# Kernel optimization log

Measured on AMD Instinct MI355X. Metric: run time of the kernel, lower is better.

Reference implementation:

```python
import jax, jax.numpy as jnp
import numpy as np

N, E, D_IN, D_H, D_OUT = 8000, 256000, 128, 128, 64
TEMP = 10.0       # config temperature.value (non-learnable)
WEIGHT = 1.0      # config weight.value (non-learnable)
LN_EPS = 1e-5


def _gcn_conv(x, W, b, src, dst, n):
    # PyG GCNConv: add self loops, sym-normalized aggregation, then bias.
    h = x @ W
    loop = jnp.arange(n)
    s = jnp.concatenate([src, loop])
    d = jnp.concatenate([dst, loop])
    deg = jnp.zeros((n,), h.dtype).at[d].add(1.0)
    dinv = jax.lax.rsqrt(jnp.maximum(deg, 1e-12))
    norm = dinv[s] * dinv[d]                       # [E+N]
    out = jax.ops.segment_sum(h[s] * norm[:, None], d, num_segments=n)
    return out + b


def _entropy_gradient(x, A, temperature, normalize):
    # E_i = 0.5 * sum_j A_ij ||x_i - x_j||^2  (dense adjacency, as in repo)
    sq = jnp.sum(x * x, axis=1)                    # [N]
    Ax = A @ x                                     # [N,d]
    deg = A.sum(axis=1)                            # [N]
    En = 0.5 * (deg * sq + A @ sq - 2.0 * jnp.sum(x * Ax, axis=1))
    if normalize:
        En = En / (jnp.max(En) + 1e-12)
    logits = -En / temperature
    P = jax.nn.softmax(logits)
    logP = jax.nn.log_softmax(logits)
    S = -jnp.sum(P * logP)
    c = P * (logP + S) / temperature               # dS/dE_k
    # dS/dx_i = c_i*(deg_i x_i - (Ax)_i) + (A^T c)_i x_i - (A^T (c*x))_i
    ATc = A.T @ c
    return (c[:, None] * (deg[:, None] * x - Ax)
            + ATc[:, None] * x - A.T @ (c[:, None] * x))


def _layer_norm(x, gamma, beta):
    mu = jnp.mean(x, axis=-1, keepdims=True)
    var = jnp.mean(jnp.square(x - mu), axis=-1, keepdims=True)
    return (x - mu) * jax.lax.rsqrt(var + LN_EPS) * gamma + beta


def setup_inputs() -> dict:
    key = jax.random.key(0)
    ks = jax.random.split(key, 6)
    def w(k, i, o):
        return jax.random.normal(k, (i, o), jnp.float32) / np.sqrt(i).astype(np.float32)
    return {
        "x": jax.random.normal(ks[0], (N, D_IN), jnp.float32),
        "edge_index": jax.random.randint(ks[1], (2, E), 0, N),
        "W1": w(ks[2], D_IN, D_H), "b1": jnp.zeros((D_H,), jnp.float32),
        "W2": w(ks[3], D_H, D_H), "b2": jnp.zeros((D_H,), jnp.float32),
        "W_out": w(ks[4], D_H, D_OUT), "b_out": jnp.zeros((D_OUT,), jnp.float32),
        "ln_gamma": jnp.ones((D_H,), jnp.float32),
        "ln_beta": jnp.zeros((D_H,), jnp.float32),
    }


def reference(x, edge_index, W1, b1, W2, b2, W_out, b_out, ln_gamma, ln_beta):
    n = x.shape[0]
    src, dst = edge_index[0], edge_index[1]
    # dense adjacency (to_dense_adj sums duplicate edges)
    A = jnp.zeros((n, n), x.dtype).at[src, dst].add(1.0)
    for W, b in ((W1, b1), (W2, b2)):
        h = _gcn_conv(x, W, b, src, dst, n)
        eg = jax.lax.stop_gradient(_entropy_gradient(h, A, TEMP, True))
        h = h + WEIGHT * eg
        h = jax.nn.relu(h)
        x = _layer_norm(h, ln_gamma, ln_beta)
    embedding = _gcn_conv(x, W_out, b_out, src, dst, n)
    return embedding
```

## Files before the change

kernel.cpp:

```cpp
#include <hip/hip_runtime.h>
#include <hip/hip_bf16.h>

#define DH 128

static constexpr float TEMP_ = 10.0f;
static constexpr float LN_EPS_ = 1e-5f;

__device__ __forceinline__ unsigned short f2bf(float f) {
  union { float f; unsigned int i; } v; v.f = f;
  unsigned int b = v.i + 0x7FFFu + ((v.i >> 16) & 1u);
  return (unsigned short)(b >> 16);
}
__device__ __forceinline__ float bf2f(unsigned short u) {
  union { unsigned int i; float f; } v; v.i = ((unsigned int)u) << 16; return v.f;
}
__device__ __forceinline__ void dec2(unsigned int u, float& lo, float& hi) {
  union { unsigned int i; float f; } a, b;
  a.i = u << 16; b.i = u & 0xFFFF0000u;
  lo = a.f; hi = b.f;
}
__device__ __forceinline__ void dec8(uint4 u, float* o) {
  dec2(u.x, o[0], o[1]); dec2(u.y, o[2], o[3]);
  dec2(u.z, o[4], o[5]); dec2(u.w, o[6], o[7]);
}
__device__ __forceinline__ unsigned int pack2(float lo, float hi) {
  return (unsigned int)f2bf(lo) | ((unsigned int)f2bf(hi) << 16);
}

__device__ __forceinline__ float grp_sum16(float v) {
  #pragma unroll
  for (int o = 8; o > 0; o >>= 1) v += __shfl_down(v, o, 16);
  return __shfl(v, 0, 16);
}

__device__ __forceinline__ float blkred(float v, bool mx, float* s4) {
  const int t = threadIdx.x;
  #pragma unroll
  for (int o = 32; o > 0; o >>= 1) {
    float u = __shfl_down(v, o, 64);
    v = mx ? fmaxf(v, u) : v + u;
  }
  __syncthreads();
  if ((t & 63) == 0) s4[t >> 6] = v;
  __syncthreads();
  float r = mx ? fmaxf(fmaxf(s4[0], s4[1]), fmaxf(s4[2], s4[3]))
               : (s4[0] + s4[1]) + (s4[2] + s4[3]);
  __syncthreads();
  return r;
}

__global__ __launch_bounds__(256) void k_gemm1_hist(const float* __restrict__ X,
                                                    const float* __restrict__ W,
                                                    unsigned short* __restrict__ Hb,
                                                    const int* __restrict__ ei, int E,
                                                    int* cnt_d, int* cnt_s, int NT) {
  __shared__ float Ws[64 * DH];
  __shared__ float xs[16 * 128];
  const int t = threadIdx.x;
  if ((int)blockIdx.x < NT) {
    const int row0 = blockIdx.x * 16;
    const float4* xg = (const float4*)(X + row0 * 128);
    float4* xs4 = (float4*)xs;
    xs4[t] = xg[t];
    xs4[t + 256] = xg[t + 256];
    const int c = t & 127, rg = t >> 7;
    float acc[8];
    #pragma unroll
    for (int r = 0; r < 8; ++r) acc[r] = 0.f;
    for (int kt = 0; kt < 2; ++kt) {
      __syncthreads();
      for (int i = t; i < 64 * DH; i += 256) Ws[i] = W[kt * 64 * DH + i];
      __syncthreads();
      for (int k = 0; k < 64; ++k) {
        float wv = Ws[k * DH + c];
        #pragma unroll
        for (int r = 0; r < 8; ++r)
          acc[r] += xs[(rg * 8 + r) * 128 + kt * 64 + k] * wv;
      }
    }
    #pragma unroll
    for (int r = 0; r < 8; ++r)
      Hb[(row0 + rg * 8 + r) * DH + c] = f2bf(acc[r]);
  } else {
    const int nb = gridDim.x - NT;
    for (int e = (blockIdx.x - NT) * 256 + t; e < E; e += nb * 256) {
      atomicAdd(&cnt_s[ei[e]], 1);
      atomicAdd(&cnt_d[ei[E + e]], 1);
    }
  }
}

__global__ __launch_bounds__(256) void k_scan_a(const int* __restrict__ cnt_d,
                                                const int* __restrict__ cnt_s,
                                                int* off_d, int* off_s, int* bsum,
                                                float* dinv, float* dego, int n) {
  __shared__ int ws4[4];
  const int t = threadIdx.x;
  const int dir = blockIdx.x >> 5, blk = blockIdx.x & 31;
  const int* cnt = dir ? cnt_s : cnt_d;
  int* off = dir ? off_s : off_d;
  const int NPB = (n + 31) >> 5;
  const int i = blk * NPB + t;
  const bool valid = (t < NPB) && (i < n);
  int tot = valid ? cnt[i] : 0;
  const int lane = t & 63, w = t >> 6;
  int v = tot;
  #pragma unroll
  for (int o = 1; o < 64; o <<= 1) {
    int u = __shfl_up(v, o, 64);
    if (lane >= o) v += u;
  }
  if (lane == 63) ws4[w] = v;
  __syncthreads();
  int wbase = 0;
  #pragma unroll
  for (int k = 0; k < 4; ++k) wbase += (k < w) ? ws4[k] : 0;
  const int excl = wbase + v - tot;
  if (valid) {
    off[i] = excl;
    if (dir == 0) dinv[i] = rsqrtf((float)tot + 1.0f);
    else          dego[i] = (float)tot;
  }
  if (t == 0) {
    int bt = 0;
    #pragma unroll
    for (int k = 0; k < 4; ++k) bt += ws4[k];
    bsum[dir * 32 + blk] = bt;
  }
}

__global__ __launch_bounds__(256) void k_scan_b(int* cnt_d, int* cnt_s,
                                                int* off_d, int* off_s,
                                                const int* __restrict__ bsum, int n) {
  __shared__ int sb;
  const int t = threadIdx.x;
  const int dir = blockIdx.x >> 5, blk = blockIdx.x & 31;
  int* cnt = dir ? cnt_s : cnt_d;
  int* off = dir ? off_s : off_d;
  if (t == 0) {
    int s = 0;
    for (int k = 0; k < blk; ++k) s += bsum[dir * 32 + k];
    sb = s;
  }
  __syncthreads();
  const int bbase = sb;
  const int NPB = (n + 31) >> 5;
  const int i = blk * NPB + t;
  if (t < NPB && i < n) {
    off[i] = bbase + off[i];
    cnt[i] = 0;
  }
  if (t == 1 && blk == 31) {
    int s = 0;
    for (int k = 0; k < 32; ++k) s += bsum[dir * 32 + k];
    off[n] = s;
  }
}

__global__ void k_fill(const int* __restrict__ ei, int E,
                       const int* __restrict__ off_d, const int* __restrict__ off_s,
                       int* cnt_d, int* cnt_s, int* idx_d, int* idx_s) {
  int e = blockIdx.x * blockDim.x + threadIdx.x;
  if (e < E) {
    int s = ei[e], d = ei[E + e];
    int p = atomicAdd(&cnt_d[d], 1);
    idx_d[off_d[d] + p] = s;
    int q = atomicAdd(&cnt_s[s], 1);
    idx_s[off_s[s] + q] = d;
  }
}

__global__ __launch_bounds__(256) void k_conv_agg(const unsigned short* __restrict__ Hb,
                                                  const float* __restrict__ dinv,
                                                  const float* __restrict__ b,
                                                  const int* __restrict__ off_d,
                                                  const int* __restrict__ idx_d,
                                                  float* __restrict__ G,
                                                  unsigned short* __restrict__ Gb,
                                                  float* __restrict__ sq) {
  const int lane = threadIdx.x & 15;
  const int i = blockIdx.x * 16 + (threadIdx.x >> 4);
  const uint4* Hv = (const uint4*)Hb;
  const float di = dinv[i];
  float acc[8];
  {
    float t8[8]; dec8(Hv[i * 16 + lane], t8);
    #pragma unroll
    for (int k = 0; k < 8; ++k) acc[k] = di * t8[k];
  }
  int o = off_d[i];
  const int oe = off_d[i + 1];
  for (; o + 8 <= oe; o += 8) {
    int s[8]; float dv[8]; uint4 r[8];
    #pragma unroll
    for (int j = 0; j < 8; ++j) s[j] = idx_d[o + j];
    #pragma unroll
    for (int j = 0; j < 8; ++j) { r[j] = Hv[s[j] * 16 + lane]; dv[j] = dinv[s[j]]; }
    #pragma unroll
    for (int j = 0; j < 8; ++j) {
      float t8[8]; dec8(r[j], t8);
      #pragma unroll
      for (int k = 0; k < 8; ++k) acc[k] = fmaf(dv[j], t8[k], acc[k]);
    }
  }
  for (; o < oe; ++o) {
    int s = idx_d[o];
    float dvs = dinv[s];
    float t8[8]; dec8(Hv[s * 16 + lane], t8);
    #pragma unroll
    for (int k = 0; k < 8; ++k) acc[k] = fmaf(dvs, t8[k], acc[k]);
  }
  const float4 b0 = ((const float4*)b)[lane * 2];
  const float4 b1 = ((const float4*)b)[lane * 2 + 1];
  float gi[8];
  gi[0] = fmaf(di, acc[0], b0.x); gi[1] = fmaf(di, acc[1], b0.y);
  gi[2] = fmaf(di, acc[2], b0.z); gi[3] = fmaf(di, acc[3], b0.w);
  gi[4] = fmaf(di, acc[4], b1.x); gi[5] = fmaf(di, acc[5], b1.y);
  gi[6] = fmaf(di, acc[6], b1.z); gi[7] = fmaf(di, acc[7], b1.w);
  ((float4*)G)[i * 32 + lane * 2]     = make_float4(gi[0], gi[1], gi[2], gi[3]);
  ((float4*)G)[i * 32 + lane * 2 + 1] = make_float4(gi[4], gi[5], gi[6], gi[7]);
  uint4 gp;
  gp.x = pack2(gi[0], gi[1]); gp.y = pack2(gi[2], gi[3]);
  gp.z = pack2(gi[4], gi[5]); gp.w = pack2(gi[6], gi[7]);
  ((uint4*)Gb)[i * 16 + lane] = gp;
  float s2 = 0.f;
  #pragma unroll
  for (int k = 0; k < 8; ++k) s2 += gi[k] * gi[k];
  s2 = grp_sum16(s2);
  if (lane == 0) sq[i] = s2;
}

__global__ __launch_bounds__(256) void k_ax_en(const float* __restrict__ G,
                                               const unsigned short* __restrict__ Gb,
                                               const float* __restrict__ sq,
                                               const float* __restrict__ dego,
                                               const int* __restrict__ off_s,
                                               const int* __restrict__ idx_s,
                                               float* __restrict__ Ax,
                                               float* __restrict__ En) {
  const int lane = threadIdx.x & 15;
  const int i = blockIdx.x * 16 + (threadIdx.x >> 4);
  const uint4* Gv = (const uint4*)Gb;
  float axf[8];
  #pragma unroll
  for (int k = 0; k < 8; ++k) axf[k] = 0.f;
  float asq = 0.f;
  int o = off_s[i];
  const int oe = off_s[i + 1];
  for (; o + 8 <= oe; o += 8) {
    int s[8]; float qv[8]; uint4 r[8];
    #pragma unroll
    for (int j = 0; j < 8; ++j) s[j] = idx_s[o + j];
    #pragma unroll
    for (int j = 0; j < 8; ++j) { r[j] = Gv[s[j] * 16 + lane]; qv[j] = sq[s[j]]; }
    #pragma unroll
    for (int j = 0; j < 8; ++j) {
      float t8[8]; dec8(r[j], t8);
      asq += qv[j];
      #pragma unroll
      for (int k = 0; k < 8; ++k) axf[k] += t8[k];
    }
  }
  for (; o < oe; ++o) {
    int s = idx_s[o];
    float t8[8]; dec8(Gv[s * 16 + lane], t8);
    asq += sq[s];
    #pragma unroll
    for (int k = 0; k < 8; ++k) axf[k] += t8[k];
  }
  ((float4*)Ax)[i * 32 + lane * 2]     = make_float4(axf[0], axf[1], axf[2], axf[3]);
  ((float4*)Ax)[i * 32 + lane * 2 + 1] = make_float4(axf[4], axf[5], axf[6], axf[7]);
  const float4 g0 = ((const float4*)G)[i * 32 + lane * 2];
  const float4 g1 = ((const float4*)G)[i * 32 + lane * 2 + 1];
  float dot = g0.x * axf[0] + g0.y * axf[1] + g0.z * axf[2] + g0.w * axf[3]
            + g1.x * axf[4] + g1.y * axf[5] + g1.z * axf[6] + g1.w * axf[7];
  dot = grp_sum16(dot);
  if (lane == 0) En[i] = 0.5f * (dego[i] * sq[i] + asq - 2.f * dot);
}

template <int DOUT>
__global__ __launch_bounds__(256) void k_combine_gemm(const float* __restrict__ G,
                                                      const unsigned short* __restrict__ Gb,
                                                      const float* __restrict__ Ax,
                                                      const float* __restrict__ En,
                                                      const float* __restrict__ dego,
                                                      const int* __restrict__ off_d,
                                                      const int* __restrict__ idx_d,
                                                      const float* __restrict__ gamma,
                                                      const float* __restrict__ beta,
                                                      const float* __restrict__ W,
                                                      unsigned short* __restrict__ Hb,
                                                      int n) {
  __shared__ unsigned short cvb[8192];
  __shared__ float Ws[32 * DOUT];
  __shared__ float xs[16 * 128];
  __shared__ float s4[4];
  const int t = threadIdx.x;

  const float4* En4 = (const float4*)En;
  const int n4 = n >> 2;
  float mloc = -3.0e38f;
  for (int k = t; k < n4; k += 256) {
    float4 e = En4[k];
    mloc = fmaxf(mloc, fmaxf(fmaxf(e.x, e.y), fmaxf(e.z, e.w)));
  }
  const float m = blkred(mloc, true, s4);
  const float invden = -1.0f / ((m + 1e-12f) * TEMP_);
  float se = 0.f, sl = 0.f;
  for (int k = t; k < n4; k += 256) {
    float4 e = En4[k];
    float l0 = e.x * invden, l1 = e.y * invden, l2 = e.z * invden, l3 = e.w * invden;
    float e0 = __expf(l0), e1 = __expf(l1), e2 = __expf(l2), e3 = __expf(l3);
    se += (e0 + e1) + (e2 + e3);
    sl += (e0 * l0 + e1 * l1) + (e2 * l2 + e3 * l3);
  }
  se = blkred(se, false, s4);
  sl = blkred(sl, false, s4);
  const float logZ = __logf(se);
  const float S = logZ - sl / se;
  const float cmul = (1.0f / se) * (1.0f / TEMP_);
  const float cadd = S - logZ;
  for (int k = t; k < n; k += 256) {
    float ls = En[k] * invden;
    cvb[k] = f2bf(__expf(ls) * cmul * (ls + cadd));
  }
  __syncthreads();

  const int lane = t & 15;
  const int i = blockIdx.x * 16 + (t >> 4);
  const uint4* Gv = (const uint4*)Gb;
  const float4 g0 = ((const float4*)G)[i * 32 + lane * 2];
  const float4 g1 = ((const float4*)G)[i * 32 + lane * 2 + 1];
  const float gi[8] = { g0.x, g0.y, g0.z, g0.w, g1.x, g1.y, g1.z, g1.w };
  float tf[8];
  #pragma unroll
  for (int k = 0; k < 8; ++k) tf[k] = 0.f;
  float atc = 0.f;
  int o = off_d[i];
  const int oe = off_d[i + 1];
  for (; o + 8 <= oe; o += 8) {
    int s[8]; float cs[8]; uint4 r[8];
    #pragma unroll
    for (int j = 0; j < 8; ++j) s[j] = idx_d[o + j];
    #pragma unroll
    for (int j = 0; j < 8; ++j) { r[j] = Gv[s[j] * 16 + lane]; cs[j] = bf2f(cvb[s[j]]); }
    #pragma unroll
    for (int j = 0; j < 8; ++j) {
      atc += cs[j];
      float t8[8]; dec8(r[j], t8);
      #pragma unroll
      for (int k = 0; k < 8; ++k) tf[k] = fmaf(cs[j], t8[k], tf[k]);
    }
  }
  for (; o < oe; ++o) {
    int s = idx_d[o];
    float cs = bf2f(cvb[s]);
    atc += cs;
    float t8[8]; dec8(Gv[s * 16 + lane], t8);
    #pragma unroll
    for (int k = 0; k < 8; ++k) tf[k] = fmaf(cs, t8[k], tf[k]);
  }
  const float ci = bf2f(cvb[i]);
  const float dg = dego[i];
  const float4 a0 = ((const float4*)Ax)[i * 32 + lane * 2];
  const float4 a1 = ((const float4*)Ax)[i * 32 + lane * 2 + 1];
  const float axi[8] = { a0.x, a0.y, a0.z, a0.w, a1.x, a1.y, a1.z, a1.w };
  float v[8];
  float ssum = 0.f;
  #pragma unroll
  for (int k = 0; k < 8; ++k) {
    v[k] = fmaxf(gi[k] + ci * (dg * gi[k] - axi[k]) + atc * gi[k] - tf[k], 0.f);
    ssum += v[k];
  }
  float mu = grp_sum16(ssum) * (1.f / 128.f);
  float vsum = 0.f;
  #pragma unroll
  for (int k = 0; k < 8; ++k) {
    v[k] -= mu;
    vsum += v[k] * v[k];
  }
  float var = grp_sum16(vsum) * (1.f / 128.f);
  float rs = rsqrtf(var + LN_EPS_);
  const float4 ga0 = ((const float4*)gamma)[lane * 2];
  const float4 ga1 = ((const float4*)gamma)[lane * 2 + 1];
  const float4 be0 = ((const float4*)beta)[lane * 2];
  const float4 be1 = ((const float4*)beta)[lane * 2 + 1];
  float4 o0, o1;
  o0.x = fmaf(v[0] * rs, ga0.x, be0.x); o0.y = fmaf(v[1] * rs, ga0.y, be0.y);
  o0.z = fmaf(v[2] * rs, ga0.z, be0.z); o0.w = fmaf(v[3] * rs, ga0.w, be0.w);
  o1.x = fmaf(v[4] * rs, ga1.x, be1.x); o1.y = fmaf(v[5] * rs, ga1.y, be1.y);
  o1.z = fmaf(v[6] * rs, ga1.z, be1.z); o1.w = fmaf(v[7] * rs, ga1.w, be1.w);

  float* xrow = xs + (t >> 4) * 128 + lane * 8;
  ((float4*)xrow)[0] = o0;
  ((float4*)xrow)[1] = o1;

  const int row0 = blockIdx.x * 16;
  constexpr int RPT = (16 * DOUT) / 256;
  const int c = t % DOUT;
  const int rg = t / DOUT;
  float acc[RPT];
  #pragma unroll
  for (int r = 0; r < RPT; ++r) acc[r] = 0.f;
  for (int kt = 0; kt < 4; ++kt) {
    if (kt) __syncthreads();
    for (int idx = t; idx < 32 * DOUT; idx += 256) Ws[idx] = W[kt * 32 * DOUT + idx];
    __syncthreads();
    for (int k = 0; k < 32; ++k) {
      float wv = Ws[k * DOUT + c];
      #pragma unroll
      for (int r = 0; r < RPT; ++r)
        acc[r] += xs[(rg * RPT + r) * 128 + kt * 32 + k] * wv;
    }
  }
  #pragma unroll
  for (int r = 0; r < RPT; ++r)
    Hb[(row0 + rg * RPT + r) * DOUT + c] = f2bf(acc[r]);
}

__global__ __launch_bounds__(256) void k_final_agg(const unsigned short* __restrict__ Hb,
                                                   const float* __restrict__ dinv,
                                                   const float* __restrict__ bout,
                                                   const int* __restrict__ off_d,
                                                   const int* __restrict__ idx_d,
                                                   float* __restrict__ out) {
  const int lane = threadIdx.x & 7;
  const int i = blockIdx.x * 32 + (threadIdx.x >> 3);
  const uint4* Hv = (const uint4*)Hb;
  const float di = dinv[i];
  float acc[8];
  {
    float t8[8]; dec8(Hv[i * 8 + lane], t8);
    #pragma unroll
    for (int k = 0; k < 8; ++k) acc[k] = di * t8[k];
  }
  int o = off_d[i];
  const int oe = off_d[i + 1];
  for (; o + 8 <= oe; o += 8) {
    int s[8]; float dv[8]; uint4 r[8];
    #pragma unroll
    for (int j = 0; j < 8; ++j) s[j] = idx_d[o + j];
    #pragma unroll
    for (int j = 0; j < 8; ++j) { r[j] = Hv[s[j] * 8 + lane]; dv[j] = dinv[s[j]]; }
    #pragma unroll
    for (int j = 0; j < 8; ++j) {
      float t8[8]; dec8(r[j], t8);
      #pragma unroll
      for (int k = 0; k < 8; ++k) acc[k] = fmaf(dv[j], t8[k], acc[k]);
    }
  }
  for (; o < oe; ++o) {
    int s = idx_d[o];
    float dvs = dinv[s];
    float t8[8]; dec8(Hv[s * 8 + lane], t8);
    #pragma unroll
    for (int k = 0; k < 8; ++k) acc[k] = fmaf(dvs, t8[k], acc[k]);
  }
  const float4 b0 = ((const float4*)bout)[lane * 2];
  const float4 b1 = ((const float4*)bout)[lane * 2 + 1];
  float4 r0, r1;
  r0.x = fmaf(di, acc[0], b0.x); r0.y = fmaf(di, acc[1], b0.y);
  r0.z = fmaf(di, acc[2], b0.z); r0.w = fmaf(di, acc[3], b0.w);
  r1.x = fmaf(di, acc[4], b1.x); r1.y = fmaf(di, acc[5], b1.y);
  r1.z = fmaf(di, acc[6], b1.z); r1.w = fmaf(di, acc[7], b1.w);
  ((float4*)out)[i * 16 + lane * 2]     = r0;
  ((float4*)out)[i * 16 + lane * 2 + 1] = r1;
}

extern "C" void kernel_launch(void* const* d_in, const int* in_sizes, int n_in,
                              void* d_out, int out_size, void* d_ws, size_t ws_size,
                              hipStream_t stream) {
  const float* x    = (const float*)d_in[0];
  const int*   ei   = (const int*)d_in[1];
  const float* W1   = (const float*)d_in[2];
  const float* b1   = (const float*)d_in[3];
  const float* W2   = (const float*)d_in[4];
  const float* b2   = (const float*)d_in[5];
  const float* Wout = (const float*)d_in[6];
  const float* bout = (const float*)d_in[7];
  const float* gam  = (const float*)d_in[8];
  const float* bet  = (const float*)d_in[9];
  float* out = (float*)d_out;

  const int N = in_sizes[0] / DH;
  const int E = in_sizes[1] / 2;

  float* ws = (float*)d_ws;
  float* G  = ws;   ws += N * DH;
  float* Ax = ws;   ws += N * DH;
  float* sq = ws;   ws += N;
  float* En = ws;   ws += N;
  float* dinv = ws; ws += N;
  float* dego = ws; ws += N;
  unsigned short* Hb = (unsigned short*)ws; ws += N * DH / 2;
  unsigned short* Gb = (unsigned short*)ws; ws += N * DH / 2;
  int* cnt_d  = (int*)ws; ws += N;
  int* cnt_s  = (int*)ws; ws += N;
  int* off_d  = (int*)ws; ws += N + 4;
  int* off_s  = (int*)ws; ws += N + 4;
  int* bsum   = (int*)ws; ws += 64;
  int* idx_d  = (int*)ws; ws += E;
  int* idx_s  = (int*)ws; ws += E;

  const int NT = N / 16;

  hipMemsetAsync(cnt_d, 0, 2 * N * sizeof(int), stream);
  k_gemm1_hist<<<NT + 256, 256, 0, stream>>>(x, W1, Hb, ei, E, cnt_d, cnt_s, NT);
  k_scan_a<<<64, 256, 0, stream>>>(cnt_d, cnt_s, off_d, off_s, bsum, dinv, dego, N);
  k_scan_b<<<64, 256, 0, stream>>>(cnt_d, cnt_s, off_d, off_s, bsum, N);
  k_fill<<<(E + 255) / 256, 256, 0, stream>>>(ei, E, off_d, off_s, cnt_d, cnt_s,
                                              idx_d, idx_s);

  k_conv_agg<<<N / 16, 256, 0, stream>>>(Hb, dinv, b1, off_d, idx_d, G, Gb, sq);
  k_ax_en<<<N / 16, 256, 0, stream>>>(G, Gb, sq, dego, off_s, idx_s, Ax, En);
  k_combine_gemm<128><<<N / 16, 256, 0, stream>>>(G, Gb, Ax, En, dego, off_d,
                                                  idx_d, gam, bet, W2, Hb, N);
  k_conv_agg<<<N / 16, 256, 0, stream>>>(Hb, dinv, b2, off_d, idx_d, G, Gb, sq);
  k_ax_en<<<N / 16, 256, 0, stream>>>(G, Gb, sq, dego, off_s, idx_s, Ax, En);
  k_combine_gemm<64><<<N / 16, 256, 0, stream>>>(G, Gb, Ax, En, dego, off_d,
                                                 idx_d, gam, bet, Wout, Hb, N);
  k_final_agg<<<N / 32, 256, 0, stream>>>(Hb, dinv, bout, off_d, idx_d, out);
}
```

Baseline: 254.8 us.

## Compute softmax entropy coefficients once in a separate kernel; shrink aggregation blocks

Before, every block of the combine-GEMM kernel recomputed the global max, softmax sums and per-node coefficients over all N energies, storing them as bf16 in shared memory. That redundant per-block reduction is moved into a single-block 1024-thread kernel that writes fp32 coefficients to a workspace array, which the combine kernel then gathers from global memory. The aggregation kernels also drop from 256- to 128-thread blocks and double their grid size, aiming for better load balance on irregular degrees. The trade-off is two extra launches and a serial single-block kernel on the critical path, plus scattered global loads of the coefficients where shared memory was used before.

```diff
diff --git a/kernel.cpp b/kernel.cpp
--- a/kernel.cpp
+++ b/kernel.cpp
@@ -11,9 +11,6 @@
   unsigned int b = v.i + 0x7FFFu + ((v.i >> 16) & 1u);
   return (unsigned short)(b >> 16);
 }
-__device__ __forceinline__ float bf2f(unsigned short u) {
-  union { unsigned int i; float f; } v; v.i = ((unsigned int)u) << 16; return v.f;
-}
 __device__ __forceinline__ void dec2(unsigned int u, float& lo, float& hi) {
   union { unsigned int i; float f; } a, b;
   a.i = u << 16; b.i = u & 0xFFFF0000u;
@@ -31,22 +28,6 @@
   #pragma unroll
   for (int o = 8; o > 0; o >>= 1) v += __shfl_down(v, o, 16);
   return __shfl(v, 0, 16);
-}
-
-__device__ __forceinline__ float blkred(float v, bool mx, float* s4) {
-  const int t = threadIdx.x;
-  #pragma unroll
-  for (int o = 32; o > 0; o >>= 1) {
-    float u = __shfl_down(v, o, 64);
-    v = mx ? fmaxf(v, u) : v + u;
-  }
-  __syncthreads();
-  if ((t & 63) == 0) s4[t >> 6] = v;
-  __syncthreads();
-  float r = mx ? fmaxf(fmaxf(s4[0], s4[1]), fmaxf(s4[2], s4[3]))
-               : (s4[0] + s4[1]) + (s4[2] + s4[3]);
-  __syncthreads();
-  return r;
 }
 
 __global__ __launch_bounds__(256) void k_gemm1_hist(const float* __restrict__ X,
@@ -170,7 +151,7 @@
   }
 }
 
-__global__ __launch_bounds__(256) void k_conv_agg(const unsigned short* __restrict__ Hb,
+__global__ __launch_bounds__(128) void k_conv_agg(const unsigned short* __restrict__ Hb,
                                                   const float* __restrict__ dinv,
                                                   const float* __restrict__ b,
                                                   const int* __restrict__ off_d,
@@ -179,7 +160,7 @@
                                                   unsigned short* __restrict__ Gb,
                                                   float* __restrict__ sq) {
   const int lane = threadIdx.x & 15;
-  const int i = blockIdx.x * 16 + (threadIdx.x >> 4);
+  const int i = blockIdx.x * 8 + (threadIdx.x >> 4);
   const uint4* Hv = (const uint4*)Hb;
   const float di = dinv[i];
   float acc[8];
@@ -230,7 +211,7 @@
   if (lane == 0) sq[i] = s2;
 }
 
-__global__ __launch_bounds__(256) void k_ax_en(const float* __restrict__ G,
+__global__ __launch_bounds__(128) void k_ax_en(const float* __restrict__ G,
                                                const unsigned short* __restrict__ Gb,
                                                const float* __restrict__ sq,
                                                const float* __restrict__ dego,
@@ -239,7 +220,7 @@
                                                float* __restrict__ Ax,
                                                float* __restrict__ En) {
   const int lane = threadIdx.x & 15;
-  const int i = blockIdx.x * 16 + (threadIdx.x >> 4);
+  const int i = blockIdx.x * 8 + (threadIdx.x >> 4);
   const uint4* Gv = (const uint4*)Gb;
   float axf[8];
   #pragma unroll
@@ -278,54 +259,66 @@
   if (lane == 0) En[i] = 0.5f * (dego[i] * sq[i] + asq - 2.f * dot);
 }
 
+__device__ __forceinline__ float red1024(float v, bool domax, float* sm) {
+  #pragma unroll
+  for (int o = 32; o > 0; o >>= 1) {
+    float u = __shfl_down(v, o, 64);
+    v = domax ? fmaxf(v, u) : v + u;
+  }
+  if ((threadIdx.x & 63) == 0) sm[threadIdx.x >> 6] = v;
+  __syncthreads();
+  if (threadIdx.x == 0) {
+    float r = sm[0];
+    for (int k = 1; k < 16; ++k) r = domax ? fmaxf(r, sm[k]) : r + sm[k];
+    sm[0] = r;
+  }
+  __syncthreads();
+  float r = sm[0];
+  __syncthreads();
+  return r;
+}
+
+__global__ __launch_bounds__(1024) void k_softc(const float* __restrict__ En,
+                                                float* __restrict__ c, int n) {
+  __shared__ float sm[16];
+  const int t = threadIdx.x;
+  float m = -1e30f;
+  for (int i = t; i < n; i += 1024) m = fmaxf(m, En[i]);
+  m = red1024(m, true, sm);
+  const float invden = -1.0f / ((m + 1e-12f) * TEMP_);
+  float se = 0.f, sl = 0.f;
+  for (int i = t; i < n; i += 1024) {
+    float li = En[i] * invden;
+    float e = __expf(li);
+    se += e; sl += e * li;
+  }
+  se = red1024(se, false, sm);
+  sl = red1024(sl, false, sm);
+  const float logZ = __logf(se);
+  const float S = logZ - sl / se;
+  const float cmul = (1.0f / se) * (1.0f / TEMP_);
+  const float cadd = S - logZ;
+  for (int i = t; i < n; i += 1024) {
+    float li = En[i] * invden;
+    c[i] = __expf(li) * cmul * (li + cadd);
+  }
+}
+
 template <int DOUT>
 __global__ __launch_bounds__(256) void k_combine_gemm(const float* __restrict__ G,
                                                       const unsigned short* __restrict__ Gb,
                                                       const float* __restrict__ Ax,
-                                                      const float* __restrict__ En,
+                                                      const float* __restrict__ cv,
                                                       const float* __restrict__ dego,
                                                       const int* __restrict__ off_d,
                                                       const int* __restrict__ idx_d,
                                                       const float* __restrict__ gamma,
                                                       const float* __restrict__ beta,
                                                       const float* __restrict__ W,
-                                                      unsigned short* __restrict__ Hb,
-                                                      int n) {
-  __shared__ unsigned short cvb[8192];
+                                                      unsigned short* __restrict__ Hb) {
   __shared__ float Ws[32 * DOUT];
   __shared__ float xs[16 * 128];
-  __shared__ float s4[4];
   const int t = threadIdx.x;
-
-  const float4* En4 = (const float4*)En;
-  const int n4 = n >> 2;
-  float mloc = -3.0e38f;
-  for (int k = t; k < n4; k += 256) {
-    float4 e = En4[k];
-    mloc = fmaxf(mloc, fmaxf(fmaxf(e.x, e.y), fmaxf(e.z, e.w)));
-  }
-  const float m = blkred(mloc, true, s4);
-  const float invden = -1.0f / ((m + 1e-12f) * TEMP_);
-  float se = 0.f, sl = 0.f;
-  for (int k = t; k < n4; k += 256) {
-    float4 e = En4[k];
-    float l0 = e.x * invden, l1 = e.y * invden, l2 = e.z * invden, l3 = e.w * invden;
-    float e0 = __expf(l0), e1 = __expf(l1), e2 = __expf(l2), e3 = __expf(l3);
-    se += (e0 + e1) + (e2 + e3);
-    sl += (e0 * l0 + e1 * l1) + (e2 * l2 + e3 * l3);
-  }
-  se = blkred(se, false, s4);
-  sl = blkred(sl, false, s4);
-  const float logZ = __logf(se);
-  const float S = logZ - sl / se;
-  const float cmul = (1.0f / se) * (1.0f / TEMP_);
-  const float cadd = S - logZ;
-  for (int k = t; k < n; k += 256) {
-    float ls = En[k] * invden;
-    cvb[k] = f2bf(__expf(ls) * cmul * (ls + cadd));
-  }
-  __syncthreads();
-
   const int lane = t & 15;
   const int i = blockIdx.x * 16 + (t >> 4);
   const uint4* Gv = (const uint4*)Gb;
@@ -343,7 +336,7 @@
     #pragma unroll
     for (int j = 0; j < 8; ++j) s[j] = idx_d[o + j];
     #pragma unroll
-    for (int j = 0; j < 8; ++j) { r[j] = Gv[s[j] * 16 + lane]; cs[j] = bf2f(cvb[s[j]]); }
+    for (int j = 0; j < 8; ++j) { r[j] = Gv[s[j] * 16 + lane]; cs[j] = cv[s[j]]; }
     #pragma unroll
     for (int j = 0; j < 8; ++j) {
       atc += cs[j];
@@ -354,13 +347,13 @@
   }
   for (; o < oe; ++o) {
     int s = idx_d[o];
-    float cs = bf2f(cvb[s]);
+    float cs = cv[s];
     atc += cs;
     float t8[8]; dec8(Gv[s * 16 + lane], t8);
     #pragma unroll
     for (int k = 0; k < 8; ++k) tf[k] = fmaf(cs, t8[k], tf[k]);
   }
-  const float ci = bf2f(cvb[i]);
+  const float ci = cv[i];
   const float dg = dego[i];
   const float4 a0 = ((const float4*)Ax)[i * 32 + lane * 2];
   const float4 a1 = ((const float4*)Ax)[i * 32 + lane * 2 + 1];
@@ -418,14 +411,14 @@
     Hb[(row0 + rg * RPT + r) * DOUT + c] = f2bf(acc[r]);
 }
 
-__global__ __launch_bounds__(256) void k_final_agg(const unsigned short* __restrict__ Hb,
+__global__ __launch_bounds__(128) void k_final_agg(const unsigned short* __restrict__ Hb,
                                                    const float* __restrict__ dinv,
                                                    const float* __restrict__ bout,
                                                    const int* __restrict__ off_d,
                                                    const int* __restrict__ idx_d,
                                                    float* __restrict__ out) {
   const int lane = threadIdx.x & 7;
-  const int i = blockIdx.x * 32 + (threadIdx.x >> 3);
+  const int i = blockIdx.x * 16 + (threadIdx.x >> 3);
   const uint4* Hv = (const uint4*)Hb;
   const float di = dinv[i];
   float acc[8];
@@ -490,6 +483,7 @@
   float* Ax = ws;   ws += N * DH;
   float* sq = ws;   ws += N;
   float* En = ws;   ws += N;
+  float* cv = ws;   ws += N;
   float* dinv = ws; ws += N;
   float* dego = ws; ws += N;
   unsigned short* Hb = (unsigned short*)ws; ws += N * DH / 2;
@@ -511,13 +505,15 @@
   k_fill<<<(E + 255) / 256, 256, 0, stream>>>(ei, E, off_d, off_s, cnt_d, cnt_s,
                                               idx_d, idx_s);
 
-  k_conv_agg<<<N / 16, 256, 0, stream>>>(Hb, dinv, b1, off_d, idx_d, G, Gb, sq);
-  k_ax_en<<<N / 16, 256, 0, stream>>>(G, Gb, sq, dego, off_s, idx_s, Ax, En);
-  k_combine_gemm<128><<<N / 16, 256, 0, stream>>>(G, Gb, Ax, En, dego, off_d,
-                                                  idx_d, gam, bet, W2, Hb, N);
-  k_conv_agg<<<N / 16, 256, 0, stream>>>(Hb, dinv, b2, off_d, idx_d, G, Gb, sq);
-  k_ax_en<<<N / 16, 256, 0, stream>>>(G, Gb, sq, dego, off_s, idx_s, Ax, En);
-  k_combine_gemm<64><<<N / 16, 256, 0, stream>>>(G, Gb, Ax, En, dego, off_d,
-                                                 idx_d, gam, bet, Wout, Hb, N);
-  k_final_agg<<<N / 32, 256, 0, stream>>>(Hb, dinv, bout, off_d, idx_d, out);
-}
+  k_conv_agg<<<N / 8, 128, 0, stream>>>(Hb, dinv, b1, off_d, idx_d, G, Gb, sq);
+  k_ax_en<<<N / 8, 128, 0, stream>>>(G, Gb, sq, dego, off_s, idx_s, Ax, En);
+  k_softc<<<1, 1024, 0, stream>>>(En, cv, N);
+  k_combine_gemm<128><<<N / 16, 256, 0, stream>>>(G, Gb, Ax, cv, dego, off_d,
+                                                  idx_d, gam, bet, W2, Hb);
+  k_conv_agg<<<N / 8, 128, 0, stream>>>(Hb, dinv, b2, off_d, idx_d, G, Gb, sq);
+  k_ax_en<<<N / 8, 128, 0, stream>>>(G, Gb, sq, dego, off_s, idx_s, Ax, En);
+  k_softc<<<1, 1024, 0, stream>>>(En, cv, N);
+  k_combine_gemm<64><<<N / 16, 256, 0, stream>>>(G, Gb, Ax, cv, dego, off_d,
+                                                 idx_d, gam, bet, Wout, Hb);
+  k_final_agg<<<N / 16, 128, 0, stream>>>(Hb, dinv, bout, off_d, idx_d, out);
+}
```

Measured after the change: 247.8 us. 1.03x faster.
